# Performance work log

Hardware: AMD Instinct MI355X
Metric: run time of the kernel (lower is better)

## Reference

```python
import jax, jax.numpy as jnp
import numpy as np

D_MODEL, D_K, D_V = 1024, 64, 64
B, S = 4, 2048

def setup_inputs() -> dict:
    key = jax.random.key(0)
    ks = jax.random.split(key, 9)
    lim = 1.0 / np.sqrt(D_MODEL)
    return {
        "query": jax.random.normal(ks[0], (B, S, D_MODEL), jnp.float32),
        "key":   jax.random.normal(ks[1], (B, S, D_MODEL), jnp.float32),
        "value": jax.random.normal(ks[2], (B, S, D_MODEL), jnp.float32),
        "Wq": jax.random.uniform(ks[3], (D_MODEL, D_K), jnp.float32, -lim, lim),
        "bq": jax.random.uniform(ks[4], (D_K,), jnp.float32, -lim, lim),
        "Wk": jax.random.uniform(ks[5], (D_MODEL, D_K), jnp.float32, -lim, lim),
        "bk": jax.random.uniform(ks[6], (D_K,), jnp.float32, -lim, lim),
        "Wv": jax.random.uniform(ks[7], (D_MODEL, D_V), jnp.float32, -lim, lim),
        "bv": jax.random.uniform(ks[8], (D_V,), jnp.float32, -lim, lim),
    }

def reference(query, key, value, Wq, bq, Wk, bk, Wv, bv):
    # Linear projections: [B,S,d_model] -> [B,S,d_k/d_v]
    q = jnp.einsum("bsd,dk->bsk", query, Wq) + bq
    k = jnp.einsum("bsd,dk->bsk", key, Wk) + bk
    v = jnp.einsum("bsd,dv->bsv", value, Wv) + bv
    scale = 1.0 / jnp.sqrt(jnp.asarray(q.shape[-1], q.dtype))
    scores = jnp.einsum("bqk,bsk->bqs", q, k) * scale  # [B,S,S]
    attn = jax.nn.softmax(scores, axis=-1)
    return jnp.einsum("bqs,bsv->bqv", attn, v)  # [B,S,d_v]
```

## Files before the change

kernel.cpp:

```cpp
#include <hip/hip_runtime.h>
#include <hip/hip_bf16.h>


typedef __attribute__((ext_vector_type(8))) short bf16x8;
typedef __attribute__((ext_vector_type(4))) float f32x4;

#define MFMA16(a, b, c) __builtin_amdgcn_mfma_f32_16x16x32_bf16((a), (b), (c), 0, 0, 0)

__device__ __forceinline__ unsigned short f2bf(float x) {
    unsigned int u = __float_as_uint(x);
    u = (u + 0x7FFFu + ((u >> 16) & 1u)) >> 16;
    return (unsigned short)u;
}

__global__ __launch_bounds__(256) void prep_w(
    const float* __restrict__ Wq, const float* __restrict__ Wk,
    const float* __restrict__ Wv, unsigned short* __restrict__ Wt) {
    int idx = blockIdx.x * 256 + threadIdx.x;
    int t = idx >> 16;
    int r = idx & 0xFFFF;
    int n = r >> 10, kk = r & 1023;
    const float* W = (t == 0) ? Wq : ((t == 1) ? Wk : Wv);
    Wt[idx] = f2bf(W[kk * 64 + n]);
}

__global__ __launch_bounds__(256) void proj_kernel(
    const float* __restrict__ xq, const float* __restrict__ xk,
    const float* __restrict__ xv, const unsigned short* __restrict__ Wt,
    const float* __restrict__ bq, const float* __restrict__ bk,
    const float* __restrict__ bv, unsigned short* __restrict__ outq,
    unsigned short* __restrict__ outk, unsigned short* __restrict__ outvt) {
    const int chunk = blockIdx.x;
    const int t = chunk >> 9;
    const int rb = chunk & 511;
    const int row0 = rb * 16;
    const float* __restrict__ x = (t == 0) ? xq : ((t == 1) ? xk : xv);
    const float* __restrict__ bias = (t == 0) ? bq : ((t == 1) ? bk : bv);

    const int tid = threadIdx.x;
    const int w = tid >> 6, l = tid & 63;
    const int lo = l & 15, q4 = l >> 4;

    const float* __restrict__ xrow = x + (size_t)(row0 + lo) * 1024 + q4 * 8;
    const unsigned short* __restrict__ wrow =
        Wt + (size_t)t * 65536 + (size_t)(w * 16 + lo) * 1024 + q4 * 8;

    f32x4 acc = {0.f, 0.f, 0.f, 0.f};
#pragma unroll 8
    for (int kk = 0; kk < 32; ++kk) {
        float4 xa = *(const float4*)(xrow + kk * 32);
        float4 xb = *(const float4*)(xrow + kk * 32 + 4);
        bf16x8 bw = *(const bf16x8*)(wrow + kk * 32);
        bf16x8 av;
        av[0] = (short)f2bf(xa.x);
        av[1] = (short)f2bf(xa.y);
        av[2] = (short)f2bf(xa.z);
        av[3] = (short)f2bf(xa.w);
        av[4] = (short)f2bf(xb.x);
        av[5] = (short)f2bf(xb.y);
        av[6] = (short)f2bf(xb.z);
        av[7] = (short)f2bf(xb.w);
        acc = MFMA16(av, bw, acc);
    }

    float bb = bias[w * 16 + lo];
#pragma unroll
    for (int i = 0; i < 4; i++) acc[i] += bb;
    if (t == 0) {
        const float SC = 0.125f * 1.44269504088896340736f;
#pragma unroll
        for (int i = 0; i < 4; i++) acc[i] *= SC;
    }
    if (t < 2) {
        unsigned short* out = (t == 0) ? outq : outk;
#pragma unroll
        for (int i = 0; i < 4; i++)
            out[(size_t)(row0 + q4 * 4 + i) * 64 + w * 16 + lo] = f2bf(acc[i]);
    } else {
        int b = row0 >> 11;
        int sl = (row0 & 2047) + q4 * 4;
        int vf = w * 16 + lo;
        ushort4 h;
        h.x = f2bf(acc[0]);
        h.y = f2bf(acc[1]);
        h.z = f2bf(acc[2]);
        h.w = f2bf(acc[3]);
        *(ushort4*)&outvt[(size_t)(b * 64 + vf) * 2048 + sl] = h;
    }
}

__global__ __launch_bounds__(256) void flash_kernel(
    const unsigned short* __restrict__ q, const unsigned short* __restrict__ k,
    const unsigned short* __restrict__ vt, float* __restrict__ Opart,
    float* __restrict__ lpart) {
    const int bx = blockIdx.x;
    const int xcd = bx & 7;
    const int b = xcd >> 1;
    const int j = ((bx >> 3) << 1) | (xcd & 1);
    const int ks = j & 3;
    const int qb = j >> 2;
    const int w = threadIdx.x >> 6, l = threadIdx.x & 63;
    const int lo = l & 15, q4 = l >> 4;

    __shared__ __align__(16) unsigned short pl[4][16][72];

    const int srow = qb * 64 + w * 16;

    const unsigned short* qp = q + (size_t)(b * 2048 + srow + lo) * 64 + q4 * 8;
    bf16x8 aq0 = *(const bf16x8*)(qp);
    bf16x8 aq1 = *(const bf16x8*)(qp + 32);

    f32x4 O[4];
    for (int i = 0; i < 4; i++)
        for (int j2 = 0; j2 < 4; j2++) O[i][j2] = 0.f;
    float ll[4] = {0.f, 0.f, 0.f, 0.f};

    for (int kt = 0; kt < 8; ++kt) {
        const int kb = ks * 512 + kt * 64;
        f32x4 S[4];
        for (int i = 0; i < 4; i++)
            for (int j2 = 0; j2 < 4; j2++) S[i][j2] = 0.f;
        const unsigned short* kp = k + (size_t)(b * 2048 + kb + lo) * 64 + q4 * 8;
#pragma unroll
        for (int ct = 0; ct < 4; ++ct) {
            bf16x8 b0 = *(const bf16x8*)(kp + ct * 1024);
            bf16x8 b1 = *(const bf16x8*)(kp + ct * 1024 + 32);
            S[ct] = MFMA16(aq0, b0, S[ct]);
            S[ct] = MFMA16(aq1, b1, S[ct]);
        }
#pragma unroll
        for (int i = 0; i < 4; i++) {
#pragma unroll
            for (int ct = 0; ct < 4; ++ct) {
                float p = exp2f(S[ct][i]);
                S[ct][i] = p;
                ll[i] += p;
            }
#pragma unroll
            for (int ct = 0; ct < 4; ++ct)
                pl[w][q4 * 4 + i][ct * 16 + lo] = f2bf(S[ct][i]);
        }
        bf16x8 ap0 = *(const bf16x8*)&pl[w][lo][q4 * 8];
        bf16x8 ap1 = *(const bf16x8*)&pl[w][lo][32 + q4 * 8];
        const unsigned short* vp =
            vt + (size_t)(b * 64 + lo) * 2048 + kb + q4 * 8;
#pragma unroll
        for (int ct = 0; ct < 4; ++ct) {
            bf16x8 v0 = *(const bf16x8*)(vp + (size_t)ct * 16 * 2048);
            bf16x8 v1 = *(const bf16x8*)(vp + (size_t)ct * 16 * 2048 + 32);
            O[ct] = MFMA16(ap0, v0, O[ct]);
            O[ct] = MFMA16(ap1, v1, O[ct]);
        }
    }
    float* op = Opart + ((size_t)(b * 4 + ks) * 2048 + srow) * 64;
#pragma unroll
    for (int ct = 0; ct < 4; ++ct)
#pragma unroll
        for (int i = 0; i < 4; i++)
            op[(size_t)(q4 * 4 + i) * 64 + ct * 16 + lo] = O[ct][i];
#pragma unroll
    for (int i = 0; i < 4; i++) {
        float s = ll[i];
        s += __shfl_xor(s, 1);
        s += __shfl_xor(s, 2);
        s += __shfl_xor(s, 4);
        s += __shfl_xor(s, 8);
        if (lo == 0)
            lpart[(size_t)(b * 4 + ks) * 2048 + srow + q4 * 4 + i] = s;
    }
}

__global__ __launch_bounds__(256) void combine_kernel(
    const float* __restrict__ Opart, const float* __restrict__ lpart,
    float* __restrict__ out) {
    int idx = blockIdx.x * 256 + threadIdx.x;
    int rowi = idx >> 4;
    int v4 = (idx & 15) * 4;
    int b = rowi >> 11, s = rowi & 2047;
    float L = 0.f;
#pragma unroll
    for (int ks = 0; ks < 4; ++ks)
        L += lpart[(size_t)(b * 4 + ks) * 2048 + s];
    float inv = 1.f / L;
    float ax = 0.f, ay = 0.f, az = 0.f, aw = 0.f;
#pragma unroll
    for (int ks = 0; ks < 4; ++ks) {
        const float4 o =
            *(const float4*)&Opart[((size_t)(b * 4 + ks) * 2048 + s) * 64 + v4];
        ax += o.x;
        ay += o.y;
        az += o.z;
        aw += o.w;
    }
    float4 res = make_float4(ax * inv, ay * inv, az * inv, aw * inv);
    *(float4*)&out[(size_t)rowi * 64 + v4] = res;
}

extern "C" void kernel_launch(void* const* d_in, const int* in_sizes, int n_in,
                              void* d_out, int out_size, void* d_ws,
                              size_t ws_size, hipStream_t stream) {
    const float* xq = (const float*)d_in[0];
    const float* xk = (const float*)d_in[1];
    const float* xv = (const float*)d_in[2];
    const float* Wq = (const float*)d_in[3];
    const float* bq = (const float*)d_in[4];
    const float* Wk = (const float*)d_in[5];
    const float* bk = (const float*)d_in[6];
    const float* Wv = (const float*)d_in[7];
    const float* bv = (const float*)d_in[8];
    float* out = (float*)d_out;

    char* ws = (char*)d_ws;
    unsigned short* qb = (unsigned short*)(ws);
    unsigned short* kb = (unsigned short*)(ws + (1u << 20));
    unsigned short* vtb = (unsigned short*)(ws + (2u << 20));
    unsigned short* Wt = (unsigned short*)(ws + (3u << 20));
    float* Opart = (float*)(ws + 3538944);
    float* lpart = (float*)(ws + 11927552);

    hipLaunchKernelGGL(prep_w, dim3(768), dim3(256), 0, stream, Wq, Wk, Wv, Wt);
    hipLaunchKernelGGL(proj_kernel, dim3(1536), dim3(256), 0, stream, xq, xk, xv,
                       Wt, bq, bk, bv, qb, kb, vtb);
    hipLaunchKernelGGL(flash_kernel, dim3(512), dim3(256), 0, stream, qb, kb,
                       vtb, Opart, lpart);
    hipLaunchKernelGGL(combine_kernel, dim3(512), dim3(256), 0, stream, Opart,
                       lpart, out);
}
```

Baseline: 211.7 us.

## Stage projection input tile in LDS once and split attention keys eightfold

The projection kernel now loads each 16-row input tile once with coalesced wide loads, converts it to bf16 and stores it in shared memory. All four waves then read it from there instead of each wave re-reading and re-converting the same fp32 rows from global memory. Weight fragments are software-prefetched one step ahead. The flash kernel splits the key dimension into 8 parts instead of 4, doubling the grid to 1024 blocks for more parallelism, at the cost of twice the partial-output traffic in the combine step.

```diff
diff --git a/kernel.cpp b/kernel.cpp
--- a/kernel.cpp
+++ b/kernel.cpp
@@ -36,34 +36,56 @@
     const int row0 = rb * 16;
     const float* __restrict__ x = (t == 0) ? xq : ((t == 1) ? xk : xv);
     const float* __restrict__ bias = (t == 0) ? bq : ((t == 1) ? bk : bv);
+    const unsigned short* __restrict__ Wtt = Wt + t * 65536;
+
+    __shared__ __align__(16) unsigned short xs[16][1040];
 
     const int tid = threadIdx.x;
     const int w = tid >> 6, l = tid & 63;
     const int lo = l & 15, q4 = l >> 4;
 
-    const float* __restrict__ xrow = x + (size_t)(row0 + lo) * 1024 + q4 * 8;
-    const unsigned short* __restrict__ wrow =
-        Wt + (size_t)t * 65536 + (size_t)(w * 16 + lo) * 1024 + q4 * 8;
+    const unsigned short* wp = Wtt + (size_t)(w * 16 + lo) * 1024 + q4 * 8;
+    bf16x8 bc0 = *(const bf16x8*)(wp);
+    bf16x8 bc1 = *(const bf16x8*)(wp + 32);
+    const float bb = bias[w * 16 + lo];
+
+    {
+        const int xr = tid >> 4;
+        const int seg = tid & 15;
+        const float* base = x + (size_t)(row0 + xr) * 1024 + seg * 64;
+        float4 v[16];
+#pragma unroll
+        for (int j = 0; j < 16; ++j) v[j] = *(const float4*)(base + j * 4);
+#pragma unroll
+        for (int j = 0; j < 8; ++j) {
+            int4 d;
+            d.x = f2bf(v[2 * j].x) | ((int)f2bf(v[2 * j].y) << 16);
+            d.y = f2bf(v[2 * j].z) | ((int)f2bf(v[2 * j].w) << 16);
+            d.z = f2bf(v[2 * j + 1].x) | ((int)f2bf(v[2 * j + 1].y) << 16);
+            d.w = f2bf(v[2 * j + 1].z) | ((int)f2bf(v[2 * j + 1].w) << 16);
+            *(int4*)&xs[xr][seg * 64 + j * 8] = d;
+        }
+    }
+    __syncthreads();
 
     f32x4 acc = {0.f, 0.f, 0.f, 0.f};
-#pragma unroll 8
-    for (int kk = 0; kk < 32; ++kk) {
-        float4 xa = *(const float4*)(xrow + kk * 32);
-        float4 xb = *(const float4*)(xrow + kk * 32 + 4);
-        bf16x8 bw = *(const bf16x8*)(wrow + kk * 32);
-        bf16x8 av;
-        av[0] = (short)f2bf(xa.x);
-        av[1] = (short)f2bf(xa.y);
-        av[2] = (short)f2bf(xa.z);
-        av[3] = (short)f2bf(xa.w);
-        av[4] = (short)f2bf(xb.x);
-        av[5] = (short)f2bf(xb.y);
-        av[6] = (short)f2bf(xb.z);
-        av[7] = (short)f2bf(xb.w);
-        acc = MFMA16(av, bw, acc);
-    }
-
-    float bb = bias[w * 16 + lo];
+#pragma unroll
+    for (int kk = 0; kk < 16; ++kk) {
+        bf16x8 a0 = *(const bf16x8*)&xs[lo][kk * 64 + q4 * 8];
+        bf16x8 a1 = *(const bf16x8*)&xs[lo][kk * 64 + 32 + q4 * 8];
+        if (kk < 15) {
+            bf16x8 bn0 = *(const bf16x8*)(wp + (kk + 1) * 64);
+            bf16x8 bn1 = *(const bf16x8*)(wp + (kk + 1) * 64 + 32);
+            acc = MFMA16(a0, bc0, acc);
+            acc = MFMA16(a1, bc1, acc);
+            bc0 = bn0;
+            bc1 = bn1;
+        } else {
+            acc = MFMA16(a0, bc0, acc);
+            acc = MFMA16(a1, bc1, acc);
+        }
+    }
+
 #pragma unroll
     for (int i = 0; i < 4; i++) acc[i] += bb;
     if (t == 0) {
@@ -97,8 +119,8 @@
     const int xcd = bx & 7;
     const int b = xcd >> 1;
     const int j = ((bx >> 3) << 1) | (xcd & 1);
-    const int ks = j & 3;
-    const int qb = j >> 2;
+    const int ks = j & 7;
+    const int qb = j >> 3;
     const int w = threadIdx.x >> 6, l = threadIdx.x & 63;
     const int lo = l & 15, q4 = l >> 4;
 
@@ -115,8 +137,8 @@
         for (int j2 = 0; j2 < 4; j2++) O[i][j2] = 0.f;
     float ll[4] = {0.f, 0.f, 0.f, 0.f};
 
-    for (int kt = 0; kt < 8; ++kt) {
-        const int kb = ks * 512 + kt * 64;
+    for (int kt = 0; kt < 4; ++kt) {
+        const int kb = ks * 256 + kt * 64;
         f32x4 S[4];
         for (int i = 0; i < 4; i++)
             for (int j2 = 0; j2 < 4; j2++) S[i][j2] = 0.f;
@@ -152,7 +174,7 @@
             O[ct] = MFMA16(ap1, v1, O[ct]);
         }
     }
-    float* op = Opart + ((size_t)(b * 4 + ks) * 2048 + srow) * 64;
+    float* op = Opart + ((size_t)(b * 8 + ks) * 2048 + srow) * 64;
 #pragma unroll
     for (int ct = 0; ct < 4; ++ct)
 #pragma unroll
@@ -166,7 +188,7 @@
         s += __shfl_xor(s, 4);
         s += __shfl_xor(s, 8);
         if (lo == 0)
-            lpart[(size_t)(b * 4 + ks) * 2048 + srow + q4 * 4 + i] = s;
+            lpart[(size_t)(b * 8 + ks) * 2048 + srow + q4 * 4 + i] = s;
     }
 }
 
@@ -179,14 +201,14 @@
     int b = rowi >> 11, s = rowi & 2047;
     float L = 0.f;
 #pragma unroll
-    for (int ks = 0; ks < 4; ++ks)
-        L += lpart[(size_t)(b * 4 + ks) * 2048 + s];
+    for (int ks = 0; ks < 8; ++ks)
+        L += lpart[(size_t)(b * 8 + ks) * 2048 + s];
     float inv = 1.f / L;
     float ax = 0.f, ay = 0.f, az = 0.f, aw = 0.f;
 #pragma unroll
-    for (int ks = 0; ks < 4; ++ks) {
+    for (int ks = 0; ks < 8; ++ks) {
         const float4 o =
-            *(const float4*)&Opart[((size_t)(b * 4 + ks) * 2048 + s) * 64 + v4];
+            *(const float4*)&Opart[((size_t)(b * 8 + ks) * 2048 + s) * 64 + v4];
         ax += o.x;
         ay += o.y;
         az += o.z;
@@ -215,13 +237,13 @@
     unsigned short* kb = (unsigned short*)(ws + (1u << 20));
     unsigned short* vtb = (unsigned short*)(ws + (2u << 20));
     unsigned short* Wt = (unsigned short*)(ws + (3u << 20));
-    float* Opart = (float*)(ws + 3538944);
-    float* lpart = (float*)(ws + 11927552);
+    float* Opart = (float*)(ws + (4u << 20));
+    float* lpart = (float*)(ws + (20u << 20));
 
     hipLaunchKernelGGL(prep_w, dim3(768), dim3(256), 0, stream, Wq, Wk, Wv, Wt);
-    hipLaunchKernelGGL(proj_kernel, dim3(1536), dim3(256), 0, stream, xq, xk, xv,
-                       Wt, bq, bk, bv, qb, kb, vtb);
-    hipLaunchKernelGGL(flash_kernel, dim3(512), dim3(256), 0, stream, qb, kb,
+    hipLaunchKernelGGL(proj_kernel, dim3(1536), dim3(256), 0, stream, xq, xk,
+                       xv, Wt, bq, bk, bv, qb, kb, vtb);
+    hipLaunchKernelGGL(flash_kernel, dim3(1024), dim3(256), 0, stream, qb, kb,
                        vtb, Opart, lpart);
     hipLaunchKernelGGL(combine_kernel, dim3(512), dim3(256), 0, stream, Opart,
                        lpart, out);
```

After: 197.7 us. 6.6% less time.
